# Optimization experiments

Measured on AMD Instinct MI355X. Metric: run time of the kernel, lower is better.

## Reference

```python
import jax, jax.numpy as jnp
import numpy as np

N = 50000
NEG_SLOPE = 0.2  # PyG GATConv default negative_slope


def gat_conv(x, src, dst, W, a_src, a_dst, b, num_nodes):
    """PyG-style GATConv (concat=True, add_self_loops handled by caller).
    x: [N, Fin], src/dst: [E'] (self-loops included), W: [Fin, H*C],
    a_src/a_dst: [H, C], b: [H*C].
    """
    H, C = a_src.shape
    h = (x @ W).reshape(num_nodes, H, C)                      # [N, H, C]
    alpha_src = jnp.einsum('nhc,hc->nh', h, a_src)            # [N, H]
    alpha_dst = jnp.einsum('nhc,hc->nh', h, a_dst)            # [N, H]
    e = jax.nn.leaky_relu(alpha_src[src] + alpha_dst[dst], NEG_SLOPE)  # [E', H]
    # segment softmax over edges grouped by destination node
    m = jax.ops.segment_max(e, dst, num_segments=num_nodes)   # [N, H]
    m = jnp.where(jnp.isfinite(m), m, 0.0)
    ex = jnp.exp(e - m[dst])                                  # [E', H]
    denom = jax.ops.segment_sum(ex, dst, num_segments=num_nodes)
    alpha = ex / (denom[dst] + 1e-16)                          # [E', H]
    # weighted scatter-sum of source features to destinations
    out = jax.ops.segment_sum(alpha[:, :, None] * h[src], dst, num_segments=num_nodes)
    return out.reshape(num_nodes, H * C) + b


def setup_inputs() -> dict:
    key = jax.random.key(0)
    ks = jax.random.split(key, 10)
    Fin, Hid, Out, Hds = 128, 32, 64, 4
    E = 800000
    x = jax.random.normal(ks[0], (N, Fin), dtype=jnp.float32)
    edge_index = jax.random.randint(ks[1], (2, E), 0, N, dtype=jnp.int64)
    s1 = (1.0 / np.sqrt(Fin)).astype(np.float32) if isinstance(np.sqrt(Fin), np.ndarray) else np.float32(1.0 / np.sqrt(Fin))
    s2 = np.float32(1.0 / np.sqrt(Hid * Hds))
    return {
        'x': x,
        'edge_index': edge_index,
        'W1': jax.random.normal(ks[2], (Fin, Hds * Hid), dtype=jnp.float32) * s1,
        'att_src1': jax.random.normal(ks[3], (Hds, Hid), dtype=jnp.float32) * 0.1,
        'att_dst1': jax.random.normal(ks[4], (Hds, Hid), dtype=jnp.float32) * 0.1,
        'b1': jnp.zeros((Hds * Hid,), dtype=jnp.float32),
        'W2': jax.random.normal(ks[5], (Hds * Hid, Out), dtype=jnp.float32) * s2,
        'att_src2': jax.random.normal(ks[6], (1, Out), dtype=jnp.float32) * 0.1,
        'att_dst2': jax.random.normal(ks[7], (1, Out), dtype=jnp.float32) * 0.1,
        'b2': jnp.zeros((Out,), dtype=jnp.float32),
    }


def reference(x, edge_index, W1, att_src1, att_dst1, b1, W2, att_src2, att_dst2, b2):
    num_nodes = x.shape[0]
    loop = jnp.arange(num_nodes, dtype=edge_index.dtype)
    src = jnp.concatenate([edge_index[0], loop])  # add self-loops (PyG default)
    dst = jnp.concatenate([edge_index[1], loop])
    h = gat_conv(x, src, dst, W1, att_src1, att_dst1, b1, num_nodes)
    h = jax.nn.relu(h)
    out = gat_conv(h, src, dst, W2, att_src2, att_dst2, b2, num_nodes)
    return out
```

## Files before the change

kernel.cpp:

```cpp
#include <hip/hip_runtime.h>
#include <hip/hip_fp16.h>

#define NN 50000
#define EE 800000
#define ELL (EE + NN)
#define NSLICE 8
#define SLICE_W (NN / NSLICE)
#define LCAP 131072
#define LCNT_STRIDE 16
#define BUCK_TILE 4096

typedef _Float16 f16x8 __attribute__((ext_vector_type(8)));
typedef float f32x4 __attribute__((ext_vector_type(4)));

__device__ __forceinline__ int edge_at(const void* ei, int is64, long long idx) {
  if (is64) return (int)((const long long*)ei)[idx];
  return ((const int*)ei)[idx];
}

__device__ __forceinline__ float leaky(float x) { return x > 0.f ? x : 0.2f * x; }


__global__ void __launch_bounds__(256) zero_detect_kernel(int* __restrict__ p, int n,
                                                          const unsigned* __restrict__ ei_words,
                                                          int* __restrict__ flag) {
  if (blockIdx.x == 0 && threadIdx.x == 0) {
    unsigned acc = 0;
    for (int i = 1; i < 64; i += 2) acc |= ei_words[i];
    *flag = (acc == 0u) ? 1 : 0;
  }
  int stride = gridDim.x * blockDim.x;
  for (int i = blockIdx.x * blockDim.x + threadIdx.x; i < n; i += stride) p[i] = 0;
}


__global__ void __launch_bounds__(256) bucket_kernel(const void* __restrict__ ei,
                                                     const int* __restrict__ flag,
                                                     unsigned* __restrict__ lists,
                                                     int* __restrict__ lcnt) {
  __shared__ int hist[NSLICE];
  __shared__ int base[NSLICE];
  __shared__ int cur[NSLICE];
  int is64 = *flag;
  int t = threadIdx.x;
  if (t < NSLICE) hist[t] = 0;
  __syncthreads();
  long long i0 = (long long)blockIdx.x * BUCK_TILE;
  unsigned pk[16];
  int sl[16];
  #pragma unroll
  for (int j = 0; j < 16; ++j) {
    long long i = i0 + t + j * 256;
    int s = -1, d = -1;
    if (i < EE) {
      s = edge_at(ei, is64, i);
      d = edge_at(ei, is64, (long long)EE + i);
    } else if (i < ELL) {
      s = d = (int)(i - EE);
    }
    if ((unsigned)s < (unsigned)NN && (unsigned)d < (unsigned)NN) {
      sl[j] = d / SLICE_W;
      pk[j] = (unsigned)s | ((unsigned)d << 16);
      atomicAdd(&hist[sl[j]], 1);
    } else {
      sl[j] = -1;
    }
  }
  __syncthreads();
  if (t < NSLICE) {
    base[t] = atomicAdd(&lcnt[t * LCNT_STRIDE], hist[t]);
    cur[t] = 0;
  }
  __syncthreads();
  #pragma unroll
  for (int j = 0; j < 16; ++j) {
    if (sl[j] >= 0) {
      int pos = base[sl[j]] + atomicAdd(&cur[sl[j]], 1);
      if (pos < LCAP) lists[(sl[j] << 17) + pos] = pk[j];
    }
  }
}


__global__ void __launch_bounds__(256) count_kernel(const unsigned* __restrict__ lists,
                                                    const int* __restrict__ lcnt,
                                                    int* __restrict__ cnt) {
  int fam = blockIdx.x & (NSLICE - 1);
  int bf = blockIdx.x >> 3;
  int nf = gridDim.x >> 3;
  int n = min(lcnt[fam * LCNT_STRIDE], LCAP);
  const unsigned* lp = lists + (fam << 17);
  for (int i = bf * blockDim.x + threadIdx.x; i < n; i += nf * blockDim.x)
    atomicAdd(&cnt[lp[i] >> 16], 1);
}

__global__ void __launch_bounds__(256) scan1_kernel(const int* __restrict__ cnt,
                                                    int* __restrict__ excl,
                                                    int* __restrict__ bsum) {
  __shared__ int sh[256];
  int t = threadIdx.x;
  int base = blockIdx.x * 1024 + t * 4;
  int v0 = 0, v1 = 0, v2 = 0, v3 = 0;
  if (base + 0 < NN) v0 = cnt[base + 0];
  if (base + 1 < NN) v1 = cnt[base + 1];
  if (base + 2 < NN) v2 = cnt[base + 2];
  if (base + 3 < NN) v3 = cnt[base + 3];
  int s = v0 + v1 + v2 + v3;
  sh[t] = s;
  __syncthreads();
  for (int off = 1; off < 256; off <<= 1) {
    int x = (t >= off) ? sh[t - off] : 0;
    __syncthreads();
    sh[t] += x;
    __syncthreads();
  }
  if (t == 255) bsum[blockIdx.x] = sh[255];
  int run = sh[t] - s;
  if (base + 0 < NN) excl[base + 0] = run;
  run += v0;
  if (base + 1 < NN) excl[base + 1] = run;
  run += v1;
  if (base + 2 < NN) excl[base + 2] = run;
  run += v2;
  if (base + 3 < NN) excl[base + 3] = run;
}

__global__ void scan2_kernel(int* __restrict__ bsum, int nb) {
  if (threadIdx.x == 0 && blockIdx.x == 0) {
    int run = 0;
    for (int i = 0; i < nb; ++i) { int x = bsum[i]; bsum[i] = run; run += x; }
    bsum[nb] = run;
  }
}

__global__ void __launch_bounds__(256) scan3_kernel(int* __restrict__ row_ptr,
                                                    const int* __restrict__ bsum,
                                                    int nb) {
  int i = blockIdx.x * blockDim.x + threadIdx.x;
  if (i < NN) row_ptr[i] += bsum[i >> 10];
  if (i == 0) row_ptr[NN] = bsum[nb];
}

__global__ void __launch_bounds__(256) scatter_kernel(const unsigned* __restrict__ lists,
                                                      const int* __restrict__ lcnt,
                                                      const int* __restrict__ row_ptr,
                                                      int* __restrict__ cursor,
                                                      unsigned* __restrict__ pairs) {
  int fam = blockIdx.x & (NSLICE - 1);
  int bf = blockIdx.x >> 3;
  int nf = gridDim.x >> 3;
  int n = min(lcnt[fam * LCNT_STRIDE], LCAP);
  const unsigned* lp = lists + (fam << 17);
  for (int i = bf * blockDim.x + threadIdx.x; i < n; i += nf * blockDim.x) {
    unsigned pk = lp[i];
    int d = pk >> 16;
    int pos = row_ptr[d] + atomicAdd(&cursor[d], 1);
    if ((unsigned)pos < (unsigned)ELL) pairs[pos] = pk;
  }
}


template <int NT, int AMODE, typename TA>
__global__ void __launch_bounds__(256) gemm_mfma(const TA* __restrict__ A,
                                                 const float* __restrict__ B,
                                                 __half* __restrict__ C,
                                                 const float* __restrict__ a_srcv,
                                                 const float* __restrict__ a_dstv,
                                                 float* __restrict__ asrc_out,
                                                 float* __restrict__ adst_out,
                                                 int M) {
  constexpr int NW = NT * 16;
  __shared__ __align__(16) __half As[64][136];
  __shared__ __align__(16) __half Bt[NW][136];
  int t = threadIdx.x;

  {
    constexpr int HALF_N = NW / 2;
    constexpr int ITER = 128 * HALF_N / 256;
    #pragma unroll
    for (int i = 0; i < ITER; ++i) {
      int idx = t + i * 256;
      int k = idx / HALF_N, n0 = (idx % HALF_N) * 2;
      float2 v = *(const float2*)&B[(size_t)k * NW + n0];
      Bt[n0][k] = __float2half(v.x);
      Bt[n0 + 1][k] = __float2half(v.y);
    }
  }

  int wv = t >> 6, l = t & 63;
  int c = l & 15, rg = l >> 4;

  #pragma unroll
  for (int rt = 0; rt < 2; ++rt) {
    int row0 = (blockIdx.x * 2 + rt) * 64;
    if constexpr (sizeof(TA) == 4) {
      #pragma unroll
      for (int i = 0; i < 8; ++i) {
        int idx = t + i * 256;
        int row = idx >> 5, kq = idx & 31;
        int gr = row0 + row;
        float4 v = make_float4(0.f, 0.f, 0.f, 0.f);
        if (gr < M) v = *(const float4*)&A[(size_t)gr * 128 + kq * 4];
        __half h4[4] = {__float2half(v.x), __float2half(v.y),
                        __float2half(v.z), __float2half(v.w)};
        *(uint2*)&As[row][kq * 4] = *(uint2*)h4;
      }
    } else {
      #pragma unroll
      for (int i = 0; i < 4; ++i) {
        int idx = t + i * 256;
        int row = idx >> 4, kc = idx & 15;
        int gr = row0 + row;
        float4 raw = make_float4(0.f, 0.f, 0.f, 0.f);
        if (gr < M) raw = *(const float4*)&A[(size_t)gr * 128 + kc * 8];
        *(float4*)&As[row][kc * 8] = raw;
      }
    }
    __syncthreads();

    f32x4 acc[NT];
    #pragma unroll
    for (int ct = 0; ct < NT; ++ct) acc[ct] = (f32x4){0.f, 0.f, 0.f, 0.f};
    #pragma unroll
    for (int ks = 0; ks < 4; ++ks) {
      f16x8 af = *(const f16x8*)&As[wv * 16 + c][ks * 32 + rg * 8];
      #pragma unroll
      for (int ct = 0; ct < NT; ++ct) {
        f16x8 bf = *(const f16x8*)&Bt[ct * 16 + c][ks * 32 + rg * 8];
        acc[ct] = __builtin_amdgcn_mfma_f32_16x16x32_f16(af, bf, acc[ct], 0, 0, 0);
      }
    }

    #pragma unroll
    for (int r = 0; r < 4; ++r) {
      int grow = row0 + wv * 16 + rg * 4 + r;
      if (grow < M) {
        #pragma unroll
        for (int ct = 0; ct < NT; ++ct)
          C[(size_t)grow * NW + ct * 16 + c] = __float2half(acc[ct][r]);
      }
    }

    if constexpr (AMODE == 1) {
      float aS[8], aD[8];
      #pragma unroll
      for (int h = 0; h < 4; ++h) {
        aS[2 * h] = a_srcv[h * 32 + c];     aS[2 * h + 1] = a_srcv[h * 32 + 16 + c];
        aD[2 * h] = a_dstv[h * 32 + c];     aD[2 * h + 1] = a_dstv[h * 32 + 16 + c];
      }
      #pragma unroll
      for (int r = 0; r < 4; ++r) {
        int grow = row0 + wv * 16 + rg * 4 + r;
        #pragma unroll
        for (int h = 0; h < 4; ++h) {
          float s = acc[2 * h][r] * aS[2 * h] + acc[2 * h + 1][r] * aS[2 * h + 1];
          float d = acc[2 * h][r] * aD[2 * h] + acc[2 * h + 1][r] * aD[2 * h + 1];
          #pragma unroll
          for (int m = 1; m <= 8; m <<= 1) {
            s += __shfl_xor(s, m, 64);
            d += __shfl_xor(d, m, 64);
          }
          if (c == 0 && grow < M) {
            asrc_out[grow * 4 + h] = s;
            adst_out[grow * 4 + h] = d;
          }
        }
      }
    } else {
      float aS[NT], aD[NT];
      #pragma unroll
      for (int ct = 0; ct < NT; ++ct) {
        aS[ct] = a_srcv[ct * 16 + c];
        aD[ct] = a_dstv[ct * 16 + c];
      }
      #pragma unroll
      for (int r = 0; r < 4; ++r) {
        int grow = row0 + wv * 16 + rg * 4 + r;
        float s = 0.f, d = 0.f;
        #pragma unroll
        for (int ct = 0; ct < NT; ++ct) {
          s += acc[ct][r] * aS[ct];
          d += acc[ct][r] * aD[ct];
        }
        #pragma unroll
        for (int m = 1; m <= 8; m <<= 1) {
          s += __shfl_xor(s, m, 64);
          d += __shfl_xor(d, m, 64);
        }
        if (c == 0 && grow < M) { asrc_out[grow] = s; adst_out[grow] = d; }
      }
    }
    __syncthreads();
  }
}


__global__ void __launch_bounds__(256) agg1_fused(
    const __half* __restrict__ h,
    const int* __restrict__ row_ptr,
    const unsigned* __restrict__ pairs,
    const float* __restrict__ asrc,
    const float* __restrict__ adst,
    const float* __restrict__ b1,
    __half* __restrict__ out)
{
  int lane = threadIdx.x & 63;
  int grp = lane >> 5;
  int cl = lane & 31;
  int c0 = cl * 4;
  int myh = cl >> 3;
  int wid = (blockIdx.x * blockDim.x + threadIdx.x) >> 6;
  int nw = (gridDim.x * blockDim.x) >> 6;
  float4 bb = *(const float4*)&b1[c0];
  for (int n = wid; n < NN; n += nw) {
    int rbeg = row_ptr[n], rend = row_ptr[n + 1];
    float ad = adst[n * 4 + myh];
    float dsum = grp ? 0.f : 1e-16f;
    float a0 = 0.f, a1 = 0.f, a2 = 0.f, a3 = 0.f;
    #pragma unroll 4
    for (int e = rbeg + grp; e < rend; e += 2) {
      int s = pairs[e] & 0xFFFF;
      float wgt = __expf(leaky(asrc[s * 4 + myh] + ad));
      float2 raw = *(const float2*)&h[(size_t)s * 128 + c0];
      float2 f01 = __half22float2(__builtin_bit_cast(__half2, raw.x));
      float2 f23 = __half22float2(__builtin_bit_cast(__half2, raw.y));
      dsum += wgt;
      a0 += wgt * f01.x; a1 += wgt * f01.y;
      a2 += wgt * f23.x; a3 += wgt * f23.y;
    }
    dsum += __shfl_xor(dsum, 32, 64);
    a0 += __shfl_xor(a0, 32, 64);
    a1 += __shfl_xor(a1, 32, 64);
    a2 += __shfl_xor(a2, 32, 64);
    a3 += __shfl_xor(a3, 32, 64);
    if (lane < 32) {
      float inv = 1.f / dsum;
      __half ot[4];
      ot[0] = __float2half(fmaxf(a0 * inv + bb.x, 0.f));
      ot[1] = __float2half(fmaxf(a1 * inv + bb.y, 0.f));
      ot[2] = __float2half(fmaxf(a2 * inv + bb.z, 0.f));
      ot[3] = __float2half(fmaxf(a3 * inv + bb.w, 0.f));
      *(uint2*)&out[(size_t)n * 128 + c0] = *(uint2*)ot;
    }
  }
}

__global__ void __launch_bounds__(256) agg2_kernel(
    const __half* __restrict__ h,
    const int* __restrict__ row_ptr,
    const unsigned* __restrict__ pairs,
    const float* __restrict__ asrc,
    const float* __restrict__ adst,
    const float* __restrict__ b2,
    float* __restrict__ out)
{
  int lane = threadIdx.x & 63;
  int grp = lane >> 3;
  int cl = lane & 7;
  int c0 = cl * 8;
  int wid = (blockIdx.x * blockDim.x + threadIdx.x) >> 6;
  int nw = (gridDim.x * blockDim.x) >> 6;
  float4 bbA = *(const float4*)&b2[c0];
  float4 bbB = *(const float4*)&b2[c0 + 4];
  for (int n = wid; n < NN; n += nw) {
    int rbeg = row_ptr[n], rend = row_ptr[n + 1];
    float ad = adst[n];
    float dsum = (grp == 0) ? 1e-16f : 0.f;
    float a0 = 0.f, a1 = 0.f, a2 = 0.f, a3 = 0.f;
    float a4 = 0.f, a5 = 0.f, a6 = 0.f, a7 = 0.f;
    #pragma unroll 2
    for (int e = rbeg + grp; e < rend; e += 8) {
      int s = pairs[e] & 0xFFFF;
      float wgt = __expf(leaky(asrc[s] + ad));
      float4 raw = *(const float4*)&h[(size_t)s * 64 + c0];
      float2 f01 = __half22float2(__builtin_bit_cast(__half2, raw.x));
      float2 f23 = __half22float2(__builtin_bit_cast(__half2, raw.y));
      float2 f45 = __half22float2(__builtin_bit_cast(__half2, raw.z));
      float2 f67 = __half22float2(__builtin_bit_cast(__half2, raw.w));
      dsum += wgt;
      a0 += wgt * f01.x; a1 += wgt * f01.y;
      a2 += wgt * f23.x; a3 += wgt * f23.y;
      a4 += wgt * f45.x; a5 += wgt * f45.y;
      a6 += wgt * f67.x; a7 += wgt * f67.y;
    }
    #pragma unroll
    for (int m = 8; m <= 32; m <<= 1) {
      dsum += __shfl_xor(dsum, m, 64);
      a0 += __shfl_xor(a0, m, 64);
      a1 += __shfl_xor(a1, m, 64);
      a2 += __shfl_xor(a2, m, 64);
      a3 += __shfl_xor(a3, m, 64);
      a4 += __shfl_xor(a4, m, 64);
      a5 += __shfl_xor(a5, m, 64);
      a6 += __shfl_xor(a6, m, 64);
      a7 += __shfl_xor(a7, m, 64);
    }
    if (lane < 8) {
      float inv = 1.f / dsum;
      float4 oA = make_float4(a0 * inv + bbA.x, a1 * inv + bbA.y,
                              a2 * inv + bbA.z, a3 * inv + bbA.w);
      float4 oB = make_float4(a4 * inv + bbB.x, a5 * inv + bbB.y,
                              a6 * inv + bbB.z, a7 * inv + bbB.w);
      *(float4*)&out[(size_t)n * 64 + c0] = oA;
      *(float4*)&out[(size_t)n * 64 + c0 + 4] = oB;
    }
  }
}


extern "C" void kernel_launch(void* const* d_in, const int* in_sizes, int n_in,
                              void* d_out, int out_size, void* d_ws, size_t ws_size,
                              hipStream_t stream) {
  const float* x   = (const float*)d_in[0];
  const void*  ei  = d_in[1];
  const float* W1  = (const float*)d_in[2];
  const float* as1 = (const float*)d_in[3];
  const float* ad1 = (const float*)d_in[4];
  const float* b1  = (const float*)d_in[5];
  const float* W2  = (const float*)d_in[6];
  const float* as2 = (const float*)d_in[7];
  const float* ad2 = (const float*)d_in[8];
  const float* b2  = (const float*)d_in[9];
  float* out = (float*)d_out;

  char* w = (char*)d_ws;
  __half* h1h  = (__half*)w; w += (size_t)NN * 128 * 2;
  __half* hb2h = h1h;
  __half* h2   = (__half*)w; w += (size_t)NN * 128 * 2;
  float* asrc1 = (float*)w; w += (size_t)NN * 4 * 4;
  float* adst1 = (float*)w; w += (size_t)NN * 4 * 4;
  float* asrc2 = (float*)w; w += (size_t)NN * 4;
  float* adst2 = (float*)w; w += (size_t)NN * 4;
  int* cnt     = (int*)w;   w += (size_t)NN * 4;
  int* cursor  = (int*)w;   w += (size_t)NN * 4;
  int* lcnt    = (int*)w;   w += 512;
  int* row_ptr = (int*)w;   w += (size_t)(NN + 1) * 4;
  int* bsum    = (int*)w;   w += 256;
  int* is64    = (int*)w;   w += 256;
  unsigned* lists = (unsigned*)w; w += (size_t)NSLICE * LCAP * 4;
  unsigned* pairs = (unsigned*)w; w += (size_t)ELL * 4;

  const int NB = (NN + 1023) / 1024;
  const int MB128 = (NN + 127) / 128;
  const int BUCK_BLOCKS = (ELL + BUCK_TILE - 1) / BUCK_TILE;

  zero_detect_kernel<<<256, 256, 0, stream>>>(cnt, 2 * NN + 128, (const unsigned*)ei, is64);
  bucket_kernel<<<BUCK_BLOCKS, 256, 0, stream>>>(ei, is64, lists, lcnt);
  count_kernel<<<2048, 256, 0, stream>>>(lists, lcnt, cnt);
  scan1_kernel<<<NB, 256, 0, stream>>>(cnt, row_ptr, bsum);
  scan2_kernel<<<1, 64, 0, stream>>>(bsum, NB);
  scan3_kernel<<<(NN + 255) / 256, 256, 0, stream>>>(row_ptr, bsum, NB);

  gemm_mfma<8, 1, float><<<MB128, 256, 0, stream>>>(
      x, W1, h1h, as1, ad1, asrc1, adst1, NN);

  scatter_kernel<<<2048, 256, 0, stream>>>(lists, lcnt, row_ptr, cursor, pairs);

  agg1_fused<<<4096, 256, 0, stream>>>(h1h, row_ptr, pairs, asrc1, adst1, b1, h2);

  gemm_mfma<4, 2, __half><<<MB128, 256, 0, stream>>>(
      h2, W2, hb2h, as2, ad2, asrc2, adst2, NN);
  agg2_kernel<<<4096, 256, 0, stream>>>(hb2h, row_ptr, pairs, asrc2, adst2, b2, out);
}
```

Measured before the change: 196.1 us.

## Fuse CSR build kernels into one cooperative kernel with grid syncs

Replaces the separate zero/detect, bucket, count, three scan and scatter kernel launches with a single cooperative kernel of 256 blocks that separates phases with grid-wide syncs. The aim is to remove launch overhead and inter-kernel gaps across the seven small preprocessing kernels. The trade-off is reduced parallelism in each phase, since the grid drops from thousands of blocks to 256, plus the cost of the grid barriers. The scatter step no longer overlaps with the first GEMM and now runs before it.

```diff
diff --git a/kernel.cpp b/kernel.cpp
--- a/kernel.cpp
+++ b/kernel.cpp
@@ -1,5 +1,8 @@
 #include <hip/hip_runtime.h>
 #include <hip/hip_fp16.h>
+#include <hip/hip_cooperative_groups.h>
+
+namespace cg = cooperative_groups;
 
 #define NN 50000
 #define EE 800000
@@ -9,6 +12,7 @@
 #define LCAP 131072
 #define LCNT_STRIDE 16
 #define BUCK_TILE 4096
+#define CSR_BLOCKS 256
 
 typedef _Float16 f16x8 __attribute__((ext_vector_type(8)));
 typedef float f32x4 __attribute__((ext_vector_type(4)));
@@ -21,141 +25,142 @@
 __device__ __forceinline__ float leaky(float x) { return x > 0.f ? x : 0.2f * x; }
 
 
-__global__ void __launch_bounds__(256) zero_detect_kernel(int* __restrict__ p, int n,
-                                                          const unsigned* __restrict__ ei_words,
-                                                          int* __restrict__ flag) {
-  if (blockIdx.x == 0 && threadIdx.x == 0) {
-    unsigned acc = 0;
-    for (int i = 1; i < 64; i += 2) acc |= ei_words[i];
-    *flag = (acc == 0u) ? 1 : 0;
-  }
-  int stride = gridDim.x * blockDim.x;
-  for (int i = blockIdx.x * blockDim.x + threadIdx.x; i < n; i += stride) p[i] = 0;
-}
-
-
-__global__ void __launch_bounds__(256) bucket_kernel(const void* __restrict__ ei,
-                                                     const int* __restrict__ flag,
-                                                     unsigned* __restrict__ lists,
-                                                     int* __restrict__ lcnt) {
-  __shared__ int hist[NSLICE];
-  __shared__ int base[NSLICE];
-  __shared__ int cur[NSLICE];
-  int is64 = *flag;
-  int t = threadIdx.x;
-  if (t < NSLICE) hist[t] = 0;
-  __syncthreads();
-  long long i0 = (long long)blockIdx.x * BUCK_TILE;
-  unsigned pk[16];
-  int sl[16];
-  #pragma unroll
-  for (int j = 0; j < 16; ++j) {
-    long long i = i0 + t + j * 256;
-    int s = -1, d = -1;
-    if (i < EE) {
-      s = edge_at(ei, is64, i);
-      d = edge_at(ei, is64, (long long)EE + i);
-    } else if (i < ELL) {
-      s = d = (int)(i - EE);
-    }
-    if ((unsigned)s < (unsigned)NN && (unsigned)d < (unsigned)NN) {
-      sl[j] = d / SLICE_W;
-      pk[j] = (unsigned)s | ((unsigned)d << 16);
-      atomicAdd(&hist[sl[j]], 1);
-    } else {
-      sl[j] = -1;
-    }
-  }
-  __syncthreads();
-  if (t < NSLICE) {
-    base[t] = atomicAdd(&lcnt[t * LCNT_STRIDE], hist[t]);
-    cur[t] = 0;
-  }
-  __syncthreads();
-  #pragma unroll
-  for (int j = 0; j < 16; ++j) {
-    if (sl[j] >= 0) {
-      int pos = base[sl[j]] + atomicAdd(&cur[sl[j]], 1);
-      if (pos < LCAP) lists[(sl[j] << 17) + pos] = pk[j];
-    }
-  }
-}
-
-
-__global__ void __launch_bounds__(256) count_kernel(const unsigned* __restrict__ lists,
-                                                    const int* __restrict__ lcnt,
-                                                    int* __restrict__ cnt) {
-  int fam = blockIdx.x & (NSLICE - 1);
-  int bf = blockIdx.x >> 3;
-  int nf = gridDim.x >> 3;
-  int n = min(lcnt[fam * LCNT_STRIDE], LCAP);
-  const unsigned* lp = lists + (fam << 17);
-  for (int i = bf * blockDim.x + threadIdx.x; i < n; i += nf * blockDim.x)
-    atomicAdd(&cnt[lp[i] >> 16], 1);
-}
-
-__global__ void __launch_bounds__(256) scan1_kernel(const int* __restrict__ cnt,
-                                                    int* __restrict__ excl,
-                                                    int* __restrict__ bsum) {
+__global__ void __launch_bounds__(256) csr_coop(const void* __restrict__ ei,
+                                                unsigned* __restrict__ lists,
+                                                int* __restrict__ lcnt,
+                                                int* __restrict__ cnt,
+                                                int* __restrict__ cursor,
+                                                int* __restrict__ row_ptr,
+                                                int* __restrict__ bsum,
+                                                unsigned* __restrict__ pairs) {
+  cg::grid_group grid = cg::this_grid();
+  __shared__ int sflag;
+  __shared__ int hist[NSLICE], sbase[NSLICE], scur[NSLICE];
   __shared__ int sh[256];
   int t = threadIdx.x;
-  int base = blockIdx.x * 1024 + t * 4;
-  int v0 = 0, v1 = 0, v2 = 0, v3 = 0;
-  if (base + 0 < NN) v0 = cnt[base + 0];
-  if (base + 1 < NN) v1 = cnt[base + 1];
-  if (base + 2 < NN) v2 = cnt[base + 2];
-  if (base + 3 < NN) v3 = cnt[base + 3];
-  int s = v0 + v1 + v2 + v3;
-  sh[t] = s;
+  int b = blockIdx.x;
+  int nb_grid = gridDim.x;
+
+  if (t == 0) {
+    const unsigned* wds = (const unsigned*)ei;
+    unsigned acc = 0;
+    for (int i = 1; i < 64; i += 2) acc |= wds[i];
+    sflag = (acc == 0u) ? 1 : 0;
+  }
   __syncthreads();
-  for (int off = 1; off < 256; off <<= 1) {
-    int x = (t >= off) ? sh[t - off] : 0;
-    __syncthreads();
-    sh[t] += x;
-    __syncthreads();
-  }
-  if (t == 255) bsum[blockIdx.x] = sh[255];
-  int run = sh[t] - s;
-  if (base + 0 < NN) excl[base + 0] = run;
-  run += v0;
-  if (base + 1 < NN) excl[base + 1] = run;
-  run += v1;
-  if (base + 2 < NN) excl[base + 2] = run;
-  run += v2;
-  if (base + 3 < NN) excl[base + 3] = run;
-}
-
-__global__ void scan2_kernel(int* __restrict__ bsum, int nb) {
-  if (threadIdx.x == 0 && blockIdx.x == 0) {
+  int is64 = sflag;
+
+  for (int i = b * 256 + t; i < 2 * NN + 128; i += nb_grid * 256) cnt[i] = 0;
+  grid.sync();
+
+  for (long long tile = b; tile * BUCK_TILE < ELL; tile += nb_grid) {
+    if (t < NSLICE) hist[t] = 0;
+    __syncthreads();
+    long long i0 = tile * BUCK_TILE;
+    unsigned pk[16];
+    int sl[16];
+    #pragma unroll
+    for (int j = 0; j < 16; ++j) {
+      long long i = i0 + t + j * 256;
+      int s = -1, d = -1;
+      if (i < EE) {
+        s = edge_at(ei, is64, i);
+        d = edge_at(ei, is64, (long long)EE + i);
+      } else if (i < ELL) {
+        s = d = (int)(i - EE);
+      }
+      if ((unsigned)s < (unsigned)NN && (unsigned)d < (unsigned)NN) {
+        sl[j] = d / SLICE_W;
+        pk[j] = (unsigned)s | ((unsigned)d << 16);
+        atomicAdd(&hist[sl[j]], 1);
+      } else {
+        sl[j] = -1;
+      }
+    }
+    __syncthreads();
+    if (t < NSLICE) {
+      sbase[t] = atomicAdd(&lcnt[t * LCNT_STRIDE], hist[t]);
+      scur[t] = 0;
+    }
+    __syncthreads();
+    #pragma unroll
+    for (int j = 0; j < 16; ++j) {
+      if (sl[j] >= 0) {
+        int pos = sbase[sl[j]] + atomicAdd(&scur[sl[j]], 1);
+        if (pos < LCAP) lists[(sl[j] << 17) + pos] = pk[j];
+      }
+    }
+    __syncthreads();
+  }
+  grid.sync();
+
+  {
+    int fam = b & (NSLICE - 1);
+    int bf = b >> 3;
+    int nf = nb_grid >> 3;
+    int n = min(lcnt[fam * LCNT_STRIDE], LCAP);
+    const unsigned* lp = lists + (fam << 17);
+    for (int i = bf * 256 + t; i < n; i += nf * 256)
+      atomicAdd(&cnt[lp[i] >> 16], 1);
+  }
+  grid.sync();
+
+  if (b < (NN + 1023) / 1024) {
+    int base = b * 1024 + t * 4;
+    int v0 = 0, v1 = 0, v2 = 0, v3 = 0;
+    if (base + 0 < NN) v0 = cnt[base + 0];
+    if (base + 1 < NN) v1 = cnt[base + 1];
+    if (base + 2 < NN) v2 = cnt[base + 2];
+    if (base + 3 < NN) v3 = cnt[base + 3];
+    int s = v0 + v1 + v2 + v3;
+    sh[t] = s;
+    __syncthreads();
+    for (int off = 1; off < 256; off <<= 1) {
+      int x = (t >= off) ? sh[t - off] : 0;
+      __syncthreads();
+      sh[t] += x;
+      __syncthreads();
+    }
+    if (t == 255) bsum[b] = sh[255];
+    int run = sh[t] - s;
+    if (base + 0 < NN) row_ptr[base + 0] = run;
+    run += v0;
+    if (base + 1 < NN) row_ptr[base + 1] = run;
+    run += v1;
+    if (base + 2 < NN) row_ptr[base + 2] = run;
+    run += v2;
+    if (base + 3 < NN) row_ptr[base + 3] = run;
+  }
+  grid.sync();
+
+  if (b == 0 && t == 0) {
+    const int nbs = (NN + 1023) / 1024;
     int run = 0;
-    for (int i = 0; i < nb; ++i) { int x = bsum[i]; bsum[i] = run; run += x; }
-    bsum[nb] = run;
-  }
-}
-
-__global__ void __launch_bounds__(256) scan3_kernel(int* __restrict__ row_ptr,
-                                                    const int* __restrict__ bsum,
-                                                    int nb) {
-  int i = blockIdx.x * blockDim.x + threadIdx.x;
-  if (i < NN) row_ptr[i] += bsum[i >> 10];
-  if (i == 0) row_ptr[NN] = bsum[nb];
-}
-
-__global__ void __launch_bounds__(256) scatter_kernel(const unsigned* __restrict__ lists,
-                                                      const int* __restrict__ lcnt,
-                                                      const int* __restrict__ row_ptr,
-                                                      int* __restrict__ cursor,
-                                                      unsigned* __restrict__ pairs) {
-  int fam = blockIdx.x & (NSLICE - 1);
-  int bf = blockIdx.x >> 3;
-  int nf = gridDim.x >> 3;
-  int n = min(lcnt[fam * LCNT_STRIDE], LCAP);
-  const unsigned* lp = lists + (fam << 17);
-  for (int i = bf * blockDim.x + threadIdx.x; i < n; i += nf * blockDim.x) {
-    unsigned pk = lp[i];
-    int d = pk >> 16;
-    int pos = row_ptr[d] + atomicAdd(&cursor[d], 1);
-    if ((unsigned)pos < (unsigned)ELL) pairs[pos] = pk;
+    for (int i = 0; i < nbs; ++i) { int x = bsum[i]; bsum[i] = run; run += x; }
+    bsum[nbs] = run;
+  }
+  grid.sync();
+
+  {
+    const int nbs = (NN + 1023) / 1024;
+    for (int i = b * 256 + t; i < NN; i += nb_grid * 256)
+      row_ptr[i] += bsum[i >> 10];
+    if (b == 0 && t == 0) row_ptr[NN] = bsum[nbs];
+  }
+  grid.sync();
+
+  {
+    int fam = b & (NSLICE - 1);
+    int bf = b >> 3;
+    int nf = nb_grid >> 3;
+    int n = min(lcnt[fam * LCNT_STRIDE], LCAP);
+    const unsigned* lp = lists + (fam << 17);
+    for (int i = bf * 256 + t; i < n; i += nf * 256) {
+      unsigned pk = lp[i];
+      int d = pk >> 16;
+      int pos = row_ptr[d] + atomicAdd(&cursor[d], 1);
+      if ((unsigned)pos < (unsigned)ELL) pairs[pos] = pk;
+    }
   }
 }
 
@@ -436,25 +441,20 @@
   int* lcnt    = (int*)w;   w += 512;
   int* row_ptr = (int*)w;   w += (size_t)(NN + 1) * 4;
   int* bsum    = (int*)w;   w += 256;
-  int* is64    = (int*)w;   w += 256;
   unsigned* lists = (unsigned*)w; w += (size_t)NSLICE * LCAP * 4;
   unsigned* pairs = (unsigned*)w; w += (size_t)ELL * 4;
 
-  const int NB = (NN + 1023) / 1024;
   const int MB128 = (NN + 127) / 128;
-  const int BUCK_BLOCKS = (ELL + BUCK_TILE - 1) / BUCK_TILE;
-
-  zero_detect_kernel<<<256, 256, 0, stream>>>(cnt, 2 * NN + 128, (const unsigned*)ei, is64);
-  bucket_kernel<<<BUCK_BLOCKS, 256, 0, stream>>>(ei, is64, lists, lcnt);
-  count_kernel<<<2048, 256, 0, stream>>>(lists, lcnt, cnt);
-  scan1_kernel<<<NB, 256, 0, stream>>>(cnt, row_ptr, bsum);
-  scan2_kernel<<<1, 64, 0, stream>>>(bsum, NB);
-  scan3_kernel<<<(NN + 255) / 256, 256, 0, stream>>>(row_ptr, bsum, NB);
+
+  {
+    void* args[] = {(void*)&ei, (void*)&lists, (void*)&lcnt, (void*)&cnt,
+                    (void*)&cursor, (void*)&row_ptr, (void*)&bsum, (void*)&pairs};
+    hipLaunchCooperativeKernel((void*)csr_coop, dim3(CSR_BLOCKS), dim3(256),
+                               args, 0, stream);
+  }
 
   gemm_mfma<8, 1, float><<<MB128, 256, 0, stream>>>(
       x, W1, h1h, as1, ad1, asrc1, adst1, NN);
-
-  scatter_kernel<<<2048, 256, 0, stream>>>(lists, lcnt, row_ptr, cursor, pairs);
 
   agg1_fused<<<4096, 256, 0, stream>>>(h1h, row_ptr, pairs, asrc1, adst1, b1, h2);
 
```

Result: slower. 351.5 us (+79.2%).
